# Performance work log

Hardware: AMD Instinct MI355X
Metric: run time of the kernel (lower is better)

## Reference

```python
import jax, jax.numpy as jnp
import numpy as np

V, C, M, O, E = 100000, 64, 8, 64, 1200000


def setup_inputs() -> dict:
    key = jax.random.key(0)
    ks = jax.random.split(key, 8)
    data = jax.random.normal(ks[0], (V, C), dtype=jnp.float32)
    edge_src = jax.random.randint(ks[1], (E,), 0, V)  # receiver vertex i
    edge_dst = jax.random.randint(ks[2], (E,), 0, V)  # neighbor vertex j
    edge_weight = jax.random.uniform(ks[3], (E,), dtype=jnp.float32)  # neighbors[i,j]
    std = 0.1  # TruncatedNormal(stddev=0.1) init
    var_u = jax.random.truncated_normal(ks[4], -2.0, 2.0, (C, M), jnp.float32) * std
    var_c = jax.random.truncated_normal(ks[5], -2.0, 2.0, (M,), jnp.float32) * std
    var_w = jax.random.truncated_normal(ks[6], -2.0, 2.0, (M, C, O), jnp.float32) * std
    var_b = jax.random.truncated_normal(ks[7], -2.0, 2.0, (O,), jnp.float32) * std
    return dict(data=data, edge_src=edge_src, edge_dst=edge_dst,
                edge_weight=edge_weight, var_u=var_u, var_c=var_c,
                var_w=var_w, var_b=var_b)


def reference(data, edge_src, edge_dst, edge_weight, var_u, var_c, var_w, var_b):
    # FeaStNet feature-steered convolution, translation invariant (var_v = -var_u):
    #   q_m(i,j) = softmax_m( u_m . (x_i - x_j) + c_m )
    #   y_i = b + sum_j neighbors[i,j] * sum_m q_m(i,j) * (W_m x_j)
    num_m, out_ch = var_w.shape[0], var_w.shape[2]
    xu = data @ var_u                                   # [V, M]
    logits = xu[edge_src] - xu[edge_dst] + var_c        # [E, M]
    q = jax.nn.softmax(logits, axis=-1)                 # [E, M] per-edge soft assignment
    x_j = data[edge_dst] * edge_weight[:, None]         # [E, C] weighted neighbor features
    out = jnp.zeros((data.shape[0], out_ch), dtype=data.dtype)
    for m in range(num_m):  # small fixed loop over M=8 weight matrices
        agg = jax.ops.segment_sum(x_j * q[:, m:m + 1], edge_src,
                                  num_segments=data.shape[0])  # [V, C]
        out = out + agg @ var_w[m]                      # [V, O]
    return out + var_b
```

## Files before the change

### kernel.cpp

```cpp
#include <hip/hip_runtime.h>
#include <hip/hip_bf16.h>
#include <hip/hip_fp16.h>

#define C_DIM 64
#define M_DIM 8
#define O_DIM 64
#define KSLOT 26
#define OVF_CAP 32768

#define G1 256
#define BSHIFT 9
#define NBMAX 208
#define CAP_PB 40

typedef _Float16 h8 __attribute__((ext_vector_type(8)));
typedef float f32x4 __attribute__((ext_vector_type(4)));

union HH { __half2 h2; unsigned int u; _Float16 f2[2]; };

__device__ __forceinline__ unsigned int packh2(float a, float b) {
    HH x;
    x.f2[0] = (_Float16)a;
    x.f2[1] = (_Float16)b;
    return x.u;
}
__device__ __forceinline__ int rfl(int x) { return __builtin_amdgcn_readfirstlane(x); }

__global__ __launch_bounds__(256) void prep_kernel(
    const float* __restrict__ data, const float* __restrict__ u,
    const int* __restrict__ esrc, const int* __restrict__ edst,
    const float* __restrict__ ew, const float* __restrict__ w,
    _Float16* __restrict__ xuh, unsigned short* __restrict__ datah,
    uint2* __restrict__ pool, int* __restrict__ gpb,
    int* __restrict__ ovf_cnt, uint4* __restrict__ ovf,
    _Float16* __restrict__ bfrag, int V, int E, int nb) {
    __shared__ int fcnt[NBMAX];
    int b = blockIdx.x, t = threadIdx.x;

    if (b < G1) {
        for (int i = t; i < NBMAX; i += 256) fcnt[i] = 0;
        __syncthreads();
        int per = (E + G1 - 1) / G1;
        int eBeg = b * per;
        int eEnd = min(E, eBeg + per);
        for (int e = eBeg + t; e < eEnd; e += 256) {
            int s = esrc[e];
            int bk = s >> BSHIFT;
            uint2 rec;
            rec.x = (unsigned int)edst[e] | ((unsigned int)(s & 511) << 17);
            rec.y = __float_as_uint(ew[e]);
            int fr = atomicAdd(&fcnt[bk], 1);
            if (fr < CAP_PB) {
                pool[((size_t)bk * G1 + b) * CAP_PB + fr] = rec;
            } else {
                int oi = atomicAdd(ovf_cnt, 1);
                if (oi < OVF_CAP) {
                    uint4 o4;
                    o4.x = (unsigned int)s;
                    o4.y = rec.x & 0x1FFFFu;
                    o4.z = rec.y;
                    o4.w = 0;
                    ovf[oi] = o4;
                }
            }
        }
        __syncthreads();
        if (t < nb) {
            int fc = fcnt[t];
            gpb[t * G1 + b] = (fc < CAP_PB) ? fc : CAP_PB;
        }
        return;
    }

    if (b < G1 + 16) {
        int tt = (b - G1) * 256 + t;
        int kt = tt >> 8;
        int rem = tt & 255;
        int nt = rem >> 6;
        int lane = rem & 63;
        int quad = lane >> 4;
        int n = nt * 16 + (lane & 15);
#pragma unroll
        for (int j = 0; j < 8; ++j) {
            int k = kt * 32 + quad * 8 + j;
            bfrag[(size_t)tt * 8 + j] = (_Float16)w[k * 64 + n];
        }
        return;
    }

    int vb = b - (G1 + 16);
    int v = vb * 32 + (t >> 3), m = t & 7;
    if (v < V) {
        const float* dr = data + (size_t)v * C_DIM;
        float s = 0.f;
#pragma unroll
        for (int c = 0; c < C_DIM; ++c) s = fmaf(dr[c], u[c * M_DIM + m], s);
        xuh[(size_t)v * 8 + m] = (_Float16)s;
    }
    size_t base = (size_t)vb * 2048 + (size_t)t * 8;
    if (base + 7 < (size_t)V * C_DIM) {
        f32x4 x0 = *(const f32x4*)&data[base];
        f32x4 x1 = *(const f32x4*)&data[base + 4];
        uint4 o;
        o.x = packh2(x0[0], x0[1]);
        o.y = packh2(x0[2], x0[3]);
        o.z = packh2(x1[0], x1[1]);
        o.w = packh2(x1[2], x1[3]);
        *(uint4*)&datah[base] = o;
    }
}

__global__ __launch_bounds__(256) void place_kernel(
    const uint2* __restrict__ pool, const int* __restrict__ gpb,
    uint2* __restrict__ recs, int* __restrict__ counts,
    int* __restrict__ ovf_cnt, uint4* __restrict__ ovf, int V) {
    __shared__ uint2 lpool[128 * CAP_PB];
    __shared__ int vcnt[512];
    __shared__ int cnts[G1];
    int b = blockIdx.x, t = threadIdx.x;
    vcnt[t] = 0;
    vcnt[t + 256] = 0;
    cnts[t] = gpb[b * G1 + t];
    __syncthreads();

#pragma unroll
    for (int h = 0; h < 2; ++h) {
        const uint4* src = (const uint4*)&pool[((size_t)b * G1 + h * 128) * CAP_PB];
        uint4* dst4 = (uint4*)lpool;
#pragma unroll
        for (int k = 0; k < 10; ++k) {
            dst4[k * 256 + t] = src[k * 256 + t];
        }
        __syncthreads();
        int sec = t & 127;
        int half = t >> 7;
        int cnt = cnts[h * 128 + sec];
        int lo = half * (CAP_PB / 2);
        int hi = min(cnt, lo + (CAP_PB / 2));
        for (int k = lo; k < hi; ++k) {
            uint2 rec = lpool[sec * CAP_PB + k];
            int low = (int)(rec.x >> 17);
            int dst = (int)(rec.x & 0x1FFFFu);
            int r = atomicAdd(&vcnt[low], 1);
            int v = (b << BSHIFT) + low;
            if (r < KSLOT) {
                uint2 o;
                o.x = (unsigned int)dst;
                o.y = rec.y;
                recs[(size_t)v * KSLOT + r] = o;
            } else {
                int oi = atomicAdd(ovf_cnt, 1);
                if (oi < OVF_CAP) {
                    uint4 o4;
                    o4.x = (unsigned int)v;
                    o4.y = (unsigned int)dst;
                    o4.z = rec.y;
                    o4.w = 0;
                    ovf[oi] = o4;
                }
            }
        }
        __syncthreads();
    }

    int v0 = (b << BSHIFT) + t;
    if (v0 < V) counts[v0] = vcnt[t] < KSLOT ? vcnt[t] : KSLOT;
    int v1 = v0 + 256;
    if (v1 < V) counts[v1] = vcnt[t + 256] < KSLOT ? vcnt[t + 256] : KSLOT;
}

#define A_STRIDE 520
__global__ __launch_bounds__(256) void fused_kernel(
    const unsigned short* __restrict__ datah, const uint2* __restrict__ recs,
    const _Float16* __restrict__ xuh, const float* __restrict__ vc,
    const int* __restrict__ counts, const _Float16* __restrict__ bfragG,
    const float* __restrict__ bias, float* __restrict__ out, int V) {
    __shared__ _Float16 At[16 * A_STRIDE];
    __shared__ int ebj[4][64];
    __shared__ uint4 ebq[4][64];
    __shared__ float xscS[4][4][8];
    __shared__ int pS[4][5];
    __shared__ int oS[4][4];
    int wave = rfl(threadIdx.x >> 6);
    int lane = threadIdx.x & 63;
    int v_base = blockIdx.x * 16;
    int v0 = v_base + wave * 4;

    if (lane < 4) {
        int v = v0 + lane;
        int dd = (v < V) ? min(counts[v], KSLOT) : 0;
        oS[wave][lane] = v * KSLOT;
        pS[wave][lane + 1] = dd;
    }
    if (lane == 0) {
        pS[wave][0] = 0;
        int s = 0;
#pragma unroll
        for (int i = 1; i <= 4; ++i) {
            s += pS[wave][i];
            pS[wave][i] = s;
        }
    }
    if (lane < 32) {
        int i = lane >> 3, m = lane & 7;
        int v = v0 + i;
        float s = 0.f;
        if (v < V) s = (float)xuh[(size_t)v0 * 8 + lane] + vc[m];
        xscS[wave][i][m] = s;
    }

    HH z; z.u = 0;
    __half2 acc[4][4];
#pragma unroll
    for (int i = 0; i < 4; ++i)
#pragma unroll
        for (int k = 0; k < 4; ++k) acc[i][k] = z.h2;

    int total = rfl(pS[wave][4]);

    for (int c0 = 0; c0 < total; c0 += 64) {
        int g = c0 + lane;
        if (g < total) {
            int p1 = pS[wave][1], p2 = pS[wave][2], p3 = pS[wave][3];
            int r = (g >= p1) + (g >= p2) + (g >= p3);
            int pr = (r > 0) ? ((r > 1) ? ((r > 2) ? p3 : p2) : p1) : 0;
            int ob = oS[wave][r];
            int pos = ob + (g - pr);
            uint2 rec = recs[pos];
            int j = (int)rec.x;
            float w = __uint_as_float(rec.y);
            f32x4 xa = *(const f32x4*)&xscS[wave][r][0];
            f32x4 xb = *(const f32x4*)&xscS[wave][r][4];
            uint4 xr = *(const uint4*)&xuh[(size_t)j * 8];
            HH a2, b2, c2, d2;
            a2.u = xr.x; b2.u = xr.y; c2.u = xr.z; d2.u = xr.w;
            float lg[8];
            lg[0] = xa[0] - (float)a2.f2[0];
            lg[1] = xa[1] - (float)a2.f2[1];
            lg[2] = xa[2] - (float)b2.f2[0];
            lg[3] = xa[3] - (float)b2.f2[1];
            lg[4] = xb[0] - (float)c2.f2[0];
            lg[5] = xb[1] - (float)c2.f2[1];
            lg[6] = xb[2] - (float)d2.f2[0];
            lg[7] = xb[3] - (float)d2.f2[1];
            float mx = -1e30f;
#pragma unroll
            for (int m = 0; m < 8; ++m) mx = fmaxf(mx, lg[m]);
            float den = 0.f;
#pragma unroll
            for (int m = 0; m < 8; ++m) {
                lg[m] = __expf(lg[m] - mx);
                den += lg[m];
            }
            float inv = w / den;
#pragma unroll
            for (int m = 0; m < 8; ++m) lg[m] *= inv;
            uint4 qp;
            qp.x = packh2(lg[0], lg[1]);
            qp.y = packh2(lg[2], lg[3]);
            qp.z = packh2(lg[4], lg[5]);
            qp.w = packh2(lg[6], lg[7]);
            ebj[wave][lane] = j;
            ebq[wave][lane] = qp;
        }
#define CONSUME2(rr, qv, xsv)                                                  \
    do {                                                                       \
        HH q01, q23, q45, q67, xx;                                             \
        q01.u = (qv).x; q23.u = (qv).y;                                        \
        q45.u = (qv).z; q67.u = (qv).w;                                        \
        unsigned int xv_ = (unsigned int)(xsv);                                \
        xx.u = xv_ | (xv_ << 16);                                              \
        acc[rr][0] = __hfma2(xx.h2, q01.h2, acc[rr][0]);                       \
        acc[rr][1] = __hfma2(xx.h2, q23.h2, acc[rr][1]);                       \
        acc[rr][2] = __hfma2(xx.h2, q45.h2, acc[rr][2]);                       \
        acc[rr][3] = __hfma2(xx.h2, q67.h2, acc[rr][3]);                       \
    } while (0)
#pragma unroll
        for (int r2 = 0; r2 < 4; ++r2) {
            int pr0 = rfl(pS[wave][r2]);
            int pr1 = rfl(pS[wave][r2 + 1]);
            int lo2 = max(pr0, c0);
            int hi2 = min(pr1, c0 + 64);
            int n = hi2 - lo2;
            if (n <= 0) continue;
            int tb = lo2 - c0;
            int tt = 0;
            for (; tt + 8 <= n; tt += 8) {
                int jj[8];
                uint4 qq[8];
                unsigned short xs[8];
#pragma unroll
                for (int u = 0; u < 8; ++u) {
                    jj[u] = rfl(ebj[wave][tb + tt + u]);
                    qq[u] = ebq[wave][tb + tt + u];
                }
#pragma unroll
                for (int u = 0; u < 8; ++u) {
                    const unsigned short* xp = datah + ((size_t)jj[u] << 6);
                    xs[u] = xp[lane];
                }
#pragma unroll
                for (int u = 0; u < 8; ++u) CONSUME2(r2, qq[u], xs[u]);
            }
            for (; tt + 4 <= n; tt += 4) {
                int jj[4];
                uint4 qq[4];
                unsigned short xs[4];
#pragma unroll
                for (int u = 0; u < 4; ++u) {
                    jj[u] = rfl(ebj[wave][tb + tt + u]);
                    qq[u] = ebq[wave][tb + tt + u];
                }
#pragma unroll
                for (int u = 0; u < 4; ++u) {
                    const unsigned short* xp = datah + ((size_t)jj[u] << 6);
                    xs[u] = xp[lane];
                }
#pragma unroll
                for (int u = 0; u < 4; ++u) CONSUME2(r2, qq[u], xs[u]);
            }
            for (; tt < n; ++tt) {
                int j0 = rfl(ebj[wave][tb + tt]);
                uint4 qv = ebq[wave][tb + tt];
                const unsigned short* xp = datah + ((size_t)j0 << 6);
                unsigned short xs0 = xp[lane];
                CONSUME2(r2, qv, xs0);
            }
        }
    }

#pragma unroll
    for (int i = 0; i < 4; ++i) {
        int row = wave * 4 + i;
        HH a01, a23, a45, a67;
        a01.h2 = acc[i][0]; a23.h2 = acc[i][1];
        a45.h2 = acc[i][2]; a67.h2 = acc[i][3];
        _Float16* Ar = &At[row * A_STRIDE + lane];
        Ar[0 * 64] = a01.f2[0];
        Ar[1 * 64] = a01.f2[1];
        Ar[2 * 64] = a23.f2[0];
        Ar[3 * 64] = a23.f2[1];
        Ar[4 * 64] = a45.f2[0];
        Ar[5 * 64] = a45.f2[1];
        Ar[6 * 64] = a67.f2[0];
        Ar[7 * 64] = a67.f2[1];
    }
    __syncthreads();

    f32x4 cacc = {0.f, 0.f, 0.f, 0.f};
    int quad = lane >> 4;
    int r16 = lane & 15;
#pragma unroll
    for (int kt = 0; kt < 16; ++kt) {
        h8 a = *(const h8*)&At[r16 * A_STRIDE + kt * 32 + quad * 8];
        h8 b = *(const h8*)&bfragG[((size_t)(kt * 4 + wave) * 64 + lane) * 8];
        cacc = __builtin_amdgcn_mfma_f32_16x16x32_f16(a, b, cacc, 0, 0, 0);
    }
#pragma unroll
    for (int r = 0; r < 4; ++r) {
        int row = quad * 4 + r;
        int v = v_base + row;
        if (v < V) {
            int o = wave * 16 + r16;
            out[(size_t)v * 64 + o] = cacc[r] + bias[o];
        }
    }
}

__global__ __launch_bounds__(256) void cleanup_kernel(
    const int* __restrict__ ovf_cnt, const uint4* __restrict__ ovf,
    const _Float16* __restrict__ xuh, const float* __restrict__ vc,
    const float* __restrict__ var_w, const unsigned short* __restrict__ datah,
    float* __restrict__ out) {
    int n = min(*ovf_cnt, OVF_CAP);
    int nw = gridDim.x * (blockDim.x >> 6);
    int wid = blockIdx.x * (blockDim.x >> 6) + (threadIdx.x >> 6);
    int lane = threadIdx.x & 63;
    for (int i = wid; i < n; i += nw) {
        uint4 r4 = ovf[i];
        int s = (int)r4.x, j = (int)r4.y;
        float w = __uint_as_float(r4.z);
        float lg[8];
        float mx = -1e30f;
#pragma unroll
        for (int m = 0; m < 8; ++m) {
            lg[m] = (float)xuh[(size_t)s * 8 + m] - (float)xuh[(size_t)j * 8 + m] + vc[m];
            mx = fmaxf(mx, lg[m]);
        }
        float den = 0.f;
#pragma unroll
        for (int m = 0; m < 8; ++m) {
            lg[m] = __expf(lg[m] - mx);
            den += lg[m];
        }
        float inv = w / den;
        float t = 0.f;
#pragma unroll
        for (int m = 0; m < 8; ++m) {
            float sum = 0.f;
            for (int c = 0; c < C_DIM; ++c) {
                HH x;
                x.u = (unsigned int)datah[(size_t)j * 64 + c];
                sum = fmaf((float)x.f2[0], var_w[((size_t)m * 64 + c) * 64 + lane], sum);
            }
            t = fmaf(lg[m] * inv, sum, t);
        }
        atomicAdd(&out[(size_t)s * 64 + lane], t);
    }
}

extern "C" void kernel_launch(void* const* d_in, const int* in_sizes, int n_in,
                              void* d_out, int out_size, void* d_ws, size_t ws_size,
                              hipStream_t stream) {
    const float* data  = (const float*)d_in[0];
    const int*   esrc  = (const int*)d_in[1];
    const int*   edst  = (const int*)d_in[2];
    const float* ew    = (const float*)d_in[3];
    const float* var_u = (const float*)d_in[4];
    const float* var_c = (const float*)d_in[5];
    const float* var_w = (const float*)d_in[6];
    const float* var_b = (const float*)d_in[7];
    float* out = (float*)d_out;

    int V = in_sizes[0] / C_DIM;
    int E = in_sizes[1];
    int nb = (V + 511) >> BSHIFT;

    char* ws = (char*)d_ws;
    size_t off = 0;
    auto alloc = [&](size_t bytes) -> void* {
        void* p = ws + off;
        off = (off + bytes + 255) & ~(size_t)255;
        return p;
    };
    int* ovf_cnt = (int*)alloc(256);

    _Float16*  xuh   = (_Float16*)alloc((size_t)V * 8 * 2);
    uint4*     ovf   = (uint4*)alloc((size_t)OVF_CAP * 16);
    uint2*     recs  = (uint2*)alloc((size_t)V * KSLOT * 8);
    _Float16*  bfrag = (_Float16*)alloc((size_t)512 * 64 * 2);
    unsigned short* datah = (unsigned short*)alloc((size_t)V * 64 * 2);
    uint2*     pool  = (uint2*)alloc((size_t)nb * G1 * CAP_PB * 8);
    int*       gpb   = (int*)alloc((size_t)nb * G1 * 4);
    int*       counts = (int*)alloc((size_t)V * 4);

    hipMemsetAsync(ovf_cnt, 0, 256, stream);

    int sb = (V * C_DIM + 2047) >> 11;
    int xb = (V + 31) >> 5;
    int streamb = sb > xb ? sb : xb;
    int g1 = G1 + 16 + streamb;
    prep_kernel<<<g1, 256, 0, stream>>>(data, var_u, esrc, edst, ew, var_w,
                                        xuh, datah, pool, gpb, ovf_cnt, ovf,
                                        bfrag, V, E, nb);
    place_kernel<<<nb, 256, 0, stream>>>(pool, gpb, recs, counts, ovf_cnt, ovf, V);
    fused_kernel<<<(V + 15) / 16, 256, 0, stream>>>(datah, recs, xuh, var_c,
                                                    counts, bfrag, var_b, out, V);
    cleanup_kernel<<<64, 256, 0, stream>>>(ovf_cnt, ovf, xuh, var_c, var_w,
                                           datah, out);
}
```

Baseline: 208.6 us.

## Halve bucket size, reshape binning grid, compute xu from coalesced loads

The edge binning uses 256-vertex buckets with 192 binning blocks and a 26-record capacity per block-bucket pair. Each place block now loads its whole pool slice at once and processes one segment per thread, giving twice as many smaller place blocks. The per-vertex xu projection now reuses the fp16-conversion loads: each thread does a partial 8x8 product from a shared-memory copy of u, then reduces across 8 lanes with shuffles. This removes strided per-thread reads of data rows. Smaller per-block capacities may push more edges into the overflow path while OVF_CAP is halved, risking dropped edges.

```diff
diff --git a/kernel.cpp b/kernel.cpp
--- a/kernel.cpp
+++ b/kernel.cpp
@@ -6,12 +6,12 @@
 #define M_DIM 8
 #define O_DIM 64
 #define KSLOT 26
-#define OVF_CAP 32768
-
-#define G1 256
-#define BSHIFT 9
-#define NBMAX 208
-#define CAP_PB 40
+#define OVF_CAP 16384
+
+#define G1 192
+#define BSHIFT 8
+#define NBMAX 400
+#define CAP_PB 26
 
 typedef _Float16 h8 __attribute__((ext_vector_type(8)));
 typedef float f32x4 __attribute__((ext_vector_type(4)));
@@ -35,10 +35,11 @@
     int* __restrict__ ovf_cnt, uint4* __restrict__ ovf,
     _Float16* __restrict__ bfrag, int V, int E, int nb) {
     __shared__ int fcnt[NBMAX];
+    __shared__ float uS[576];
     int b = blockIdx.x, t = threadIdx.x;
 
     if (b < G1) {
-        for (int i = t; i < NBMAX; i += 256) fcnt[i] = 0;
+        for (int i = t; i < nb; i += 256) fcnt[i] = 0;
         __syncthreads();
         int per = (E + G1 - 1) / G1;
         int eBeg = b * per;
@@ -47,7 +48,7 @@
             int s = esrc[e];
             int bk = s >> BSHIFT;
             uint2 rec;
-            rec.x = (unsigned int)edst[e] | ((unsigned int)(s & 511) << 17);
+            rec.x = (unsigned int)edst[e] | ((unsigned int)(s & 255) << 17);
             rec.y = __float_as_uint(ew[e]);
             int fr = atomicAdd(&fcnt[bk], 1);
             if (fr < CAP_PB) {
@@ -65,9 +66,9 @@
             }
         }
         __syncthreads();
-        if (t < nb) {
-            int fc = fcnt[t];
-            gpb[t * G1 + b] = (fc < CAP_PB) ? fc : CAP_PB;
+        for (int i = t; i < nb; i += 256) {
+            int fc = fcnt[i];
+            gpb[i * G1 + b] = (fc < CAP_PB) ? fc : CAP_PB;
         }
         return;
     }
@@ -89,15 +90,11 @@
     }
 
     int vb = b - (G1 + 16);
-    int v = vb * 32 + (t >> 3), m = t & 7;
-    if (v < V) {
-        const float* dr = data + (size_t)v * C_DIM;
-        float s = 0.f;
-#pragma unroll
-        for (int c = 0; c < C_DIM; ++c) s = fmaf(dr[c], u[c * M_DIM + m], s);
-        xuh[(size_t)v * 8 + m] = (_Float16)s;
-    }
+    for (int i = t; i < 512; i += 256) uS[(i >> 3) * 9 + (i & 7)] = u[i];
+    __syncthreads();
+
     size_t base = (size_t)vb * 2048 + (size_t)t * 8;
+    float x[8];
     if (base + 7 < (size_t)V * C_DIM) {
         f32x4 x0 = *(const f32x4*)&data[base];
         f32x4 x1 = *(const f32x4*)&data[base + 4];
@@ -107,6 +104,34 @@
         o.z = packh2(x1[0], x1[1]);
         o.w = packh2(x1[2], x1[3]);
         *(uint4*)&datah[base] = o;
+        x[0] = x0[0]; x[1] = x0[1]; x[2] = x0[2]; x[3] = x0[3];
+        x[4] = x1[0]; x[5] = x1[1]; x[6] = x1[2]; x[7] = x1[3];
+    } else {
+#pragma unroll
+        for (int i = 0; i < 8; ++i) x[i] = 0.f;
+    }
+    int c0 = (t & 7) * 8;
+    float p[8];
+#pragma unroll
+    for (int m = 0; m < 8; ++m) p[m] = 0.f;
+#pragma unroll
+    for (int i = 0; i < 8; ++i) {
+        const float* ur = &uS[(c0 + i) * 9];
+#pragma unroll
+        for (int m = 0; m < 8; ++m) p[m] = fmaf(x[i], ur[m], p[m]);
+    }
+#pragma unroll
+    for (int d = 1; d < 8; d <<= 1) {
+#pragma unroll
+        for (int m = 0; m < 8; ++m) p[m] += __shfl_xor(p[m], d, 64);
+    }
+    int v = vb * 32 + (t >> 3);
+    if (v < V) {
+        int mi = t & 7;
+        float outv = p[0];
+#pragma unroll
+        for (int m = 1; m < 8; ++m) if (mi == m) outv = p[m];
+        xuh[(size_t)v * 8 + mi] = (_Float16)outv;
     }
 }
 
@@ -114,31 +139,24 @@
     const uint2* __restrict__ pool, const int* __restrict__ gpb,
     uint2* __restrict__ recs, int* __restrict__ counts,
     int* __restrict__ ovf_cnt, uint4* __restrict__ ovf, int V) {
-    __shared__ uint2 lpool[128 * CAP_PB];
-    __shared__ int vcnt[512];
+    __shared__ uint2 lpool[G1 * CAP_PB];
+    __shared__ int vcnt[256];
     __shared__ int cnts[G1];
     int b = blockIdx.x, t = threadIdx.x;
     vcnt[t] = 0;
-    vcnt[t + 256] = 0;
-    cnts[t] = gpb[b * G1 + t];
+    if (t < G1) cnts[t] = gpb[b * G1 + t];
+    const uint4* src = (const uint4*)&pool[(size_t)b * G1 * CAP_PB];
+    uint4* dst4 = (uint4*)lpool;
+    for (int i = t; i < G1 * CAP_PB / 2; i += 256) dst4[i] = src[i];
     __syncthreads();
 
-#pragma unroll
-    for (int h = 0; h < 2; ++h) {
-        const uint4* src = (const uint4*)&pool[((size_t)b * G1 + h * 128) * CAP_PB];
-        uint4* dst4 = (uint4*)lpool;
-#pragma unroll
-        for (int k = 0; k < 10; ++k) {
-            dst4[k * 256 + t] = src[k * 256 + t];
-        }
-        __syncthreads();
-        int sec = t & 127;
-        int half = t >> 7;
-        int cnt = cnts[h * 128 + sec];
-        int lo = half * (CAP_PB / 2);
-        int hi = min(cnt, lo + (CAP_PB / 2));
-        for (int k = lo; k < hi; ++k) {
-            uint2 rec = lpool[sec * CAP_PB + k];
+    if (t < G1) {
+        int cnt = cnts[t];
+        if (cnt > CAP_PB) cnt = CAP_PB;
+        if (cnt < 0) cnt = 0;
+        int basei = t * CAP_PB;
+        for (int k = 0; k < cnt; ++k) {
+            uint2 rec = lpool[basei + k];
             int low = (int)(rec.x >> 17);
             int dst = (int)(rec.x & 0x1FFFFu);
             int r = atomicAdd(&vcnt[low], 1);
@@ -160,13 +178,10 @@
                 }
             }
         }
-        __syncthreads();
-    }
-
+    }
+    __syncthreads();
     int v0 = (b << BSHIFT) + t;
     if (v0 < V) counts[v0] = vcnt[t] < KSLOT ? vcnt[t] : KSLOT;
-    int v1 = v0 + 256;
-    if (v1 < V) counts[v1] = vcnt[t + 256] < KSLOT ? vcnt[t + 256] : KSLOT;
 }
 
 #define A_STRIDE 520
@@ -424,7 +439,7 @@
 
     int V = in_sizes[0] / C_DIM;
     int E = in_sizes[1];
-    int nb = (V + 511) >> BSHIFT;
+    int nb = (V + 255) >> BSHIFT;
 
     char* ws = (char*)d_ws;
     size_t off = 0;
@@ -447,9 +462,7 @@
     hipMemsetAsync(ovf_cnt, 0, 256, stream);
 
     int sb = (V * C_DIM + 2047) >> 11;
-    int xb = (V + 31) >> 5;
-    int streamb = sb > xb ? sb : xb;
-    int g1 = G1 + 16 + streamb;
+    int g1 = G1 + 16 + sb;
     prep_kernel<<<g1, 256, 0, stream>>>(data, var_u, esrc, edst, ew, var_w,
                                         xuh, datah, pool, gpb, ovf_cnt, ovf,
                                         bfrag, V, E, nb);
```

New measurement: 246.4 us. 18.1% more time.

## Pack edge records into 32 bits with fp16 weight and widen place kernel

Applied to the files above, without the earlier changes.

Edge records stored per receiver are compressed from 8 bytes (index + fp32 weight) to 4 bytes (17-bit neighbor index plus 15-bit fp16 weight without sign), halving record write and read traffic between the placement and fused kernels. The placement kernel now runs 512 threads and stages the whole block's pool into shared memory in one pass instead of two halves, removing a sync phase. This reduces weight precision to fp16, assumes nonnegative weights, and increases shared memory use per block.

```diff
diff --git a/kernel.cpp b/kernel.cpp
--- a/kernel.cpp
+++ b/kernel.cpp
@@ -110,44 +110,44 @@
     }
 }
 
-__global__ __launch_bounds__(256) void place_kernel(
+__global__ __launch_bounds__(512) void place_kernel(
     const uint2* __restrict__ pool, const int* __restrict__ gpb,
-    uint2* __restrict__ recs, int* __restrict__ counts,
+    unsigned int* __restrict__ recs, int* __restrict__ counts,
     int* __restrict__ ovf_cnt, uint4* __restrict__ ovf, int V) {
-    __shared__ uint2 lpool[128 * CAP_PB];
+    __shared__ uint2 lpool[G1 * CAP_PB];
     __shared__ int vcnt[512];
     __shared__ int cnts[G1];
     int b = blockIdx.x, t = threadIdx.x;
     vcnt[t] = 0;
-    vcnt[t + 256] = 0;
-    cnts[t] = gpb[b * G1 + t];
+    if (t < G1) cnts[t] = gpb[b * G1 + t];
+    const uint4* src = (const uint4*)&pool[(size_t)b * G1 * CAP_PB];
+    uint4* dst4 = (uint4*)lpool;
+#pragma unroll
+    for (int k = 0; k < G1 * CAP_PB / 2 / 512; ++k) {
+        dst4[k * 512 + t] = src[k * 512 + t];
+    }
     __syncthreads();
 
-#pragma unroll
-    for (int h = 0; h < 2; ++h) {
-        const uint4* src = (const uint4*)&pool[((size_t)b * G1 + h * 128) * CAP_PB];
-        uint4* dst4 = (uint4*)lpool;
-#pragma unroll
-        for (int k = 0; k < 10; ++k) {
-            dst4[k * 256 + t] = src[k * 256 + t];
-        }
-        __syncthreads();
-        int sec = t & 127;
-        int half = t >> 7;
-        int cnt = cnts[h * 128 + sec];
+    {
+        int sec = t >> 1;
+        int half = t & 1;
+        int cnt = cnts[sec];
+        if (cnt > CAP_PB) cnt = CAP_PB;
+        if (cnt < 0) cnt = 0;
         int lo = half * (CAP_PB / 2);
-        int hi = min(cnt, lo + (CAP_PB / 2));
+        int hi = half ? cnt : min(cnt, CAP_PB / 2);
+        int basei = sec * CAP_PB;
         for (int k = lo; k < hi; ++k) {
-            uint2 rec = lpool[sec * CAP_PB + k];
+            uint2 rec = lpool[basei + k];
             int low = (int)(rec.x >> 17);
             int dst = (int)(rec.x & 0x1FFFFu);
             int r = atomicAdd(&vcnt[low], 1);
             int v = (b << BSHIFT) + low;
             if (r < KSLOT) {
-                uint2 o;
-                o.x = (unsigned int)dst;
-                o.y = rec.y;
-                recs[(size_t)v * KSLOT + r] = o;
+                HH wh;
+                wh.f2[0] = (_Float16)__uint_as_float(rec.y);
+                unsigned int wf = wh.u & 0xFFFFu;
+                recs[(size_t)v * KSLOT + r] = (unsigned int)dst | (wf << 17);
             } else {
                 int oi = atomicAdd(ovf_cnt, 1);
                 if (oi < OVF_CAP) {
@@ -160,18 +160,15 @@
                 }
             }
         }
-        __syncthreads();
-    }
-
+    }
+    __syncthreads();
     int v0 = (b << BSHIFT) + t;
     if (v0 < V) counts[v0] = vcnt[t] < KSLOT ? vcnt[t] : KSLOT;
-    int v1 = v0 + 256;
-    if (v1 < V) counts[v1] = vcnt[t + 256] < KSLOT ? vcnt[t + 256] : KSLOT;
 }
 
 #define A_STRIDE 520
 __global__ __launch_bounds__(256) void fused_kernel(
-    const unsigned short* __restrict__ datah, const uint2* __restrict__ recs,
+    const unsigned short* __restrict__ datah, const unsigned int* __restrict__ recs,
     const _Float16* __restrict__ xuh, const float* __restrict__ vc,
     const int* __restrict__ counts, const _Float16* __restrict__ bfragG,
     const float* __restrict__ bias, float* __restrict__ out, int V) {
@@ -226,9 +223,10 @@
             int pr = (r > 0) ? ((r > 1) ? ((r > 2) ? p3 : p2) : p1) : 0;
             int ob = oS[wave][r];
             int pos = ob + (g - pr);
-            uint2 rec = recs[pos];
-            int j = (int)rec.x;
-            float w = __uint_as_float(rec.y);
+            unsigned int rec = recs[pos];
+            int j = (int)(rec & 0x1FFFFu);
+            HH wh; wh.u = rec >> 17;
+            float w = (float)wh.f2[0];
             f32x4 xa = *(const f32x4*)&xscS[wave][r][0];
             f32x4 xb = *(const f32x4*)&xscS[wave][r][4];
             uint4 xr = *(const uint4*)&xuh[(size_t)j * 8];
@@ -437,7 +435,7 @@
 
     _Float16*  xuh   = (_Float16*)alloc((size_t)V * 8 * 2);
     uint4*     ovf   = (uint4*)alloc((size_t)OVF_CAP * 16);
-    uint2*     recs  = (uint2*)alloc((size_t)V * KSLOT * 8);
+    unsigned int* recs = (unsigned int*)alloc((size_t)V * KSLOT * 4);
     _Float16*  bfrag = (_Float16*)alloc((size_t)512 * 64 * 2);
     unsigned short* datah = (unsigned short*)alloc((size_t)V * 64 * 2);
     uint2*     pool  = (uint2*)alloc((size_t)nb * G1 * CAP_PB * 8);
@@ -453,7 +451,7 @@
     prep_kernel<<<g1, 256, 0, stream>>>(data, var_u, esrc, edst, ew, var_w,
                                         xuh, datah, pool, gpb, ovf_cnt, ovf,
                                         bfrag, V, E, nb);
-    place_kernel<<<nb, 256, 0, stream>>>(pool, gpb, recs, counts, ovf_cnt, ovf, V);
+    place_kernel<<<nb, 512, 0, stream>>>(pool, gpb, recs, counts, ovf_cnt, ovf, V);
     fused_kernel<<<(V + 15) / 16, 256, 0, stream>>>(datah, recs, xuh, var_c,
                                                     counts, bfrag, var_b, out, V);
     cleanup_kernel<<<64, 256, 0, stream>>>(ovf_cnt, ovf, xuh, var_c, var_w,
```

Result: no change. 209.5 us (+0.4%).
